# Optimization experiments

Hardware: AMD Instinct MI355X
Metric: run time of the kernel (lower is better)

The kernel has to match this reference:

```python
import jax, jax.numpy as jnp
import numpy as np
import math

B, S, D, H, C, A, SD, L, STEPS = 128, 256, 1024, 16, 50, 32, 64, 6, 10


def setup_inputs():
    key = jax.random.key(0)
    ks = jax.random.split(key, 16)
    rn = lambda k, sh, std=0.02: jax.random.normal(k, sh, jnp.float32) * std
    z = lambda sh: jnp.zeros(sh, jnp.float32)
    o = lambda sh: jnp.ones(sh, jnp.float32)
    return dict(
        reasoning=jax.random.normal(ks[0], (B, S, D), jnp.float32),
        state=jax.random.normal(ks[1], (B, SD), jnp.float32),
        x0=jax.random.normal(ks[2], (B, C, A), jnp.float32),
        W_se=rn(ks[3], (SD, D)), b_se=z(D), g_se=o(D), be_se=z(D),
        W_ap=rn(ks[4], (A, D)), b_ap=z(D),
        W_ad=rn(ks[5], (D, A), 0.001), b_ad=z(A),
        mem_latent=rn(ks[6], (1, 1, D)),
        Wq=rn(ks[7], (D, D)), bq=z(D), Wk=rn(ks[8], (D, D)), bk=z(D),
        Wv=rn(ks[9], (D, D)), bv=z(D), Wo=rn(ks[10], (D, D)), bo=z(D),
        g_q=o(D), be_q=z(D), g_kv=o(D), be_kv=z(D),
        W_fp=rn(ks[11], (D, D)), b_fp=z(D),
        pos_emb=rn(ks[12], (C, D)),
        filmW=rn(ks[13], (L, D, D)), filmb=z((L, D)), filmg=o((L, D)), filmbe=z((L, D)),
        filmWf=rn(ks[14], (L, D, 2 * D)), filmbf=z((L, 2 * D)),
        flow_steps=STEPS,
    )


def _ln(x, g, b):
    m = x.mean(-1, keepdims=True)
    v = jnp.mean((x - m) ** 2, -1, keepdims=True)
    return (x - m) * jax.lax.rsqrt(v + 1e-5) * g + b


def reference(reasoning, state, x0, W_se, b_se, g_se, be_se, W_ap, b_ap, W_ad, b_ad,
              mem_latent, Wq, bq, Wk, bk, Wv, bv, Wo, bo, g_q, be_q, g_kv, be_kv,
              W_fp, b_fp, pos_emb, filmW, filmb, filmg, filmbe, filmWf, filmbf, flow_steps):
    B_, C_, A_ = x0.shape
    D_ = W_ap.shape[1]
    dh = D_ // H
    # --- generate_mem: cross-attn from learned latent over [reasoning; state_enc] ---
    se = _ln(state @ W_se + b_se, g_se, be_se)[:, None, :]          # [B,1,D]
    kv = _ln(jnp.concatenate([reasoning, se], 1), g_kv, be_kv)      # [B,S+1,D]
    q = _ln(jnp.broadcast_to(mem_latent, (B_, 1, D_)), g_q, be_q)   # [B,1,D]
    qh = (q @ Wq + bq).reshape(B_, 1, H, dh)
    kh = (kv @ Wk + bk).reshape(B_, -1, H, dh)
    vh = (kv @ Wv + bv).reshape(B_, -1, H, dh)
    att = jax.nn.softmax(jnp.einsum('bqhd,bkhd->bhqk', qh, kh) / math.sqrt(dh), -1)
    mem = jnp.einsum('bhqk,bkhd->bqhd', att, vh).reshape(B_, 1, D_) @ Wo + bo
    film_vec = mem[:, 0] @ W_fp + b_fp                               # [B,D]
    cond = jnp.broadcast_to(film_vec[:, None, :], (B_, C_, D_)).reshape(B_ * C_, D_)
    half = D_ // 2
    freqs = jnp.exp(jnp.linspace(0.0, math.log(1000.0), half))

    def velocity(x_t, t):
        x = x_t @ W_ap + b_ap + pos_emb[None]                        # [B,C,D]
        targ = t[:, None] * freqs[None, :]
        temb = jnp.concatenate([jnp.sin(targ), jnp.cos(targ)], -1)   # [B,D]
        h = (x + temb[:, None, :]).reshape(B_ * C_, D_)

        def film_step(h, p):
            W, b, g, be, Wf, bf = p
            hh = _ln(h @ W + b, g, be)
            gamma, beta = jnp.split(cond @ Wf + bf, 2, -1)
            return jax.nn.gelu((1.0 + gamma) * hh + beta, approximate=False), None

        h, _ = jax.lax.scan(film_step, h, (filmW, filmb, filmg, filmbe, filmWf, filmbf))
        return (h @ W_ad + b_ad).reshape(B_, C_, A_)

    # --- flow-matching Euler integration (sample) ---
    dt = 1.0 / flow_steps
    ts = jnp.arange(flow_steps, dtype=jnp.float32) * dt

    def euler(x_t, tval):
        v = velocity(x_t, jnp.full((B_,), tval))
        return x_t + v * dt, None

    x_t, _ = jax.lax.scan(euler, x0, ts)
    return x_t
```

## Files before the change

### kernel.cpp

```cpp
#include <hip/hip_runtime.h>
#include <math.h>

#define NB 128
#define NS 256
#define ND 1024
#define NH 16
#define NC 50
#define NA 32
#define NSD 64
#define NL 6
#define NSTEPS 10
#define NM (NB*NC)
#define NKV (NS+1)

typedef unsigned short u16;
typedef short bf16x8 __attribute__((ext_vector_type(8)));
typedef float f32x4 __attribute__((ext_vector_type(4)));
typedef unsigned short us4 __attribute__((ext_vector_type(4)));
typedef unsigned short us8 __attribute__((ext_vector_type(8)));

typedef __attribute__((address_space(1))) const void* gas_p;
typedef __attribute__((address_space(3))) void* las_p;

__device__ __forceinline__ float b2f(u16 h) { return __uint_as_float(((unsigned int)h) << 16); }
__device__ __forceinline__ u16 f2b(float f) {
  unsigned int u = __float_as_uint(f);
  return (u16)((u + 0x7fffu + ((u >> 16) & 1u)) >> 16);
}
__device__ __forceinline__ void gld16(const void* g, void* l) {
  __builtin_amdgcn_global_load_lds((gas_p)g, (las_p)l, 16, 0, 0);
}

__device__ __forceinline__ float wredsum(float v) {
#pragma unroll
  for (int o = 32; o > 0; o >>= 1) v += __shfl_down(v, o, 64);
  return v;
}
__device__ __forceinline__ void bsum2(float& a, float& b, float* red, int t) {
  float ra = wredsum(a), rb = wredsum(b);
  if ((t & 63) == 0) { red[(t >> 6) * 2] = ra; red[(t >> 6) * 2 + 1] = rb; }
  __syncthreads();
  a = red[0] + red[2] + red[4] + red[6];
  b = red[1] + red[3] + red[5] + red[7];
  __syncthreads();
}

__global__ __launch_bounds__(512) void film_gemm(const u16* __restrict__ Ag,
                                                 const u16* __restrict__ Bg,
                                                 u16* __restrict__ Ug) {
  __shared__ u16 As[2][4096];
  __shared__ u16 Bs[2][4096];
  const int t = threadIdx.x, lane = t & 63, w = t >> 6;
  const int rb_ = blockIdx.x;
  const int bid = (rb_ & 7) * 50 + (rb_ >> 3);
  const int tm = bid >> 3, tn = bid & 7;
  const u16* Ab = Ag + (size_t)tm * 128 * ND;
  const u16* Bb = Bg + (size_t)tn * 128 * ND;
  const int srow = t >> 2, sq = (t & 3) * 8;
  const int wm = w >> 2, wn = w & 3;
  const int wr = wm * 64, wc = wn * 32;
  const int fr = lane & 15, fq = (lane >> 4) * 8;

  f32x4 acc[4][2];
#pragma unroll
  for (int m = 0; m < 4; ++m)
#pragma unroll
    for (int n = 0; n < 2; ++n)
#pragma unroll
      for (int j = 0; j < 4; ++j) acc[m][n][j] = 0.f;

  gld16(Ab + (size_t)srow * ND + sq, As[0] + w * 512);
  gld16(Bb + (size_t)srow * ND + sq, Bs[0] + w * 512);
  __syncthreads();

  for (int it = 0; it < 32; ++it) {
    const int cur = it & 1;
    if (it < 31) {
      const int k0 = (it + 1) * 32;
      gld16(Ab + (size_t)srow * ND + k0 + sq, As[cur ^ 1] + w * 512);
      gld16(Bb + (size_t)srow * ND + k0 + sq, Bs[cur ^ 1] + w * 512);
    }
    bf16x8 af[4], bfv[2];
#pragma unroll
    for (int m = 0; m < 4; ++m) af[m] = *(const bf16x8*)(As[cur] + (wr + m * 16 + fr) * 32 + fq);
#pragma unroll
    for (int n = 0; n < 2; ++n) bfv[n] = *(const bf16x8*)(Bs[cur] + (wc + n * 16 + fr) * 32 + fq);
#pragma unroll
    for (int m = 0; m < 4; ++m)
#pragma unroll
      for (int n = 0; n < 2; ++n)
        acc[m][n] = __builtin_amdgcn_mfma_f32_16x16x32_bf16(af[m], bfv[n], acc[m][n], 0, 0, 0);
    __syncthreads();
  }
  const int rbb = tm * 128 + wr + (lane >> 4) * 4;
  const int cbb = tn * 128 + wc + fr;
#pragma unroll
  for (int m = 0; m < 4; ++m)
#pragma unroll
    for (int n = 0; n < 2; ++n)
#pragma unroll
      for (int j = 0; j < 4; ++j)
        Ug[(size_t)(rbb + m * 16 + j) * ND + cbb + n * 16] = f2b(acc[m][n][j]);
}

__global__ __launch_bounds__(256) void bgemm(const u16* __restrict__ A, const int a_rstride,
    const int a_zoff, const u16* __restrict__ Bp, const long long b_zoff,
    const float* __restrict__ bias, const int bias_zoff, u16* __restrict__ C,
    const int c_rstride, const long long c_zoff) {
  __shared__ u16 As[4096];
  __shared__ u16 Bs[2048];
  const int t = threadIdx.x, wv = t >> 6, lane = t & 63;
  const int nt = blockIdx.x, z = blockIdx.y;
  const u16* Ab = A + (size_t)z * a_zoff;
  const u16* Bb = Bp + (size_t)z * b_zoff + (size_t)nt * 64 * ND;
  const int ca = wv * 128 + lane;
  const int ra0 = ca >> 2, qa0 = (ca & 3) * 8;
  const int ca1 = ca + 64;
  const int ra1 = ca1 >> 2, qa1 = (ca1 & 3) * 8;
  const int cbk = wv * 64 + lane;
  const int rb0 = cbk >> 2, qb0 = (cbk & 3) * 8;
  const int wr = (wv >> 1) * 64, wc = (wv & 1) * 32;
  const int fr = lane & 15, fq = (lane >> 4) * 8;

  f32x4 acc[4][2];
#pragma unroll
  for (int m = 0; m < 4; ++m)
#pragma unroll
    for (int n = 0; n < 2; ++n)
#pragma unroll
      for (int j = 0; j < 4; ++j) acc[m][n][j] = 0.f;

  for (int k0 = 0; k0 < ND; k0 += 32) {
    __syncthreads();
    gld16(Ab + (size_t)ra0 * a_rstride + k0 + qa0, As + wv * 1024);
    gld16(Ab + (size_t)ra1 * a_rstride + k0 + qa1, As + wv * 1024 + 512);
    gld16(Bb + (size_t)rb0 * ND + k0 + qb0, Bs + wv * 512);
    __syncthreads();
    bf16x8 af[4], bfv[2];
#pragma unroll
    for (int m = 0; m < 4; ++m) af[m] = *(const bf16x8*)(As + (wr + m * 16 + fr) * 32 + fq);
#pragma unroll
    for (int n = 0; n < 2; ++n) bfv[n] = *(const bf16x8*)(Bs + (wc + n * 16 + fr) * 32 + fq);
#pragma unroll
    for (int m = 0; m < 4; ++m)
#pragma unroll
      for (int n = 0; n < 2; ++n)
        acc[m][n] = __builtin_amdgcn_mfma_f32_16x16x32_bf16(af[m], bfv[n], acc[m][n], 0, 0, 0);
  }
  const int rb = wr + (lane >> 4) * 4;
#pragma unroll
  for (int n = 0; n < 2; ++n) {
    const int col = nt * 64 + wc + n * 16 + fr;
    const float bz = bias[(size_t)z * bias_zoff + col];
#pragma unroll
    for (int m = 0; m < 4; ++m)
#pragma unroll
      for (int j = 0; j < 4; ++j)
        C[(size_t)z * c_zoff + (size_t)(rb + m * 16 + j) * c_rstride + col] =
            f2b(acc[m][n][j] + bz);
  }
}

__global__ __launch_bounds__(256) void ln_film(const u16* __restrict__ U,
    const float* __restrict__ lb, const float* __restrict__ lg, const float* __restrict__ lbe,
    const u16* __restrict__ gbB, u16* __restrict__ Hout) {
  const int t = threadIdx.x, wv = t >> 6, lane = t & 63;
  const int row = blockIdx.x * 4 + wv;
  const int b = row / NC;
  const int d0 = lane * 16;
  const u16* up = U + (size_t)row * ND + d0;
  us8 u0 = *(const us8*)up;
  us8 u1 = *(const us8*)(up + 8);
  float lbv[16], lgv[16], lbev[16];
#pragma unroll
  for (int i = 0; i < 4; ++i) {
    *(f32x4*)&lbv[i * 4]  = *(const f32x4*)&lb[d0 + i * 4];
    *(f32x4*)&lgv[i * 4]  = *(const f32x4*)&lg[d0 + i * 4];
    *(f32x4*)&lbev[i * 4] = *(const f32x4*)&lbe[d0 + i * 4];
  }
  float x[16];
#pragma unroll
  for (int i = 0; i < 8; ++i) x[i] = b2f((u16)u0[i]) + lbv[i];
#pragma unroll
  for (int i = 0; i < 8; ++i) x[8 + i] = b2f((u16)u1[i]) + lbv[8 + i];
  float s = 0.f, q = 0.f;
#pragma unroll
  for (int i = 0; i < 16; ++i) { s += x[i]; q += x[i] * x[i]; }
#pragma unroll
  for (int o = 32; o > 0; o >>= 1) { s += __shfl_xor(s, o, 64); q += __shfl_xor(q, o, 64); }
  const float m = s * (1.f / ND);
  const float rstd = rsqrtf(q * (1.f / ND) - m * m + 1e-5f);
  const u16* gbb = gbB + (size_t)b * (2 * ND);
  us8 g0 = *(const us8*)(gbb + d0);
  us8 g1 = *(const us8*)(gbb + d0 + 8);
  us8 e0 = *(const us8*)(gbb + ND + d0);
  us8 e1 = *(const us8*)(gbb + ND + d0 + 8);
  us8 o0, o1;
#pragma unroll
  for (int i = 0; i < 16; ++i) {
    const float hh = (x[i] - m) * rstd * lgv[i] + lbev[i];
    const float ga = (i < 8) ? b2f((u16)g0[i]) : b2f((u16)g1[i - 8]);
    const float be = (i < 8) ? b2f((u16)e0[i]) : b2f((u16)e1[i - 8]);
    const float y = (1.f + ga) * hh + be;
    const float gl = 0.5f * y * (1.f + erff(y * 0.70710678118654752f));
    const u16 r = f2b(gl);
    if (i < 8) o0[i] = r; else o1[i - 8] = r;
  }
  u16* op = Hout + (size_t)row * ND + d0;
  *(us8*)op = o0;
  *(us8*)(op + 8) = o1;
}

__global__ __launch_bounds__(256) void h0_mfma(const float* __restrict__ X,
    const u16* __restrict__ WapP, const float* __restrict__ bt,
    const float* __restrict__ pos, u16* __restrict__ Hout) {
  __shared__ u16 As[4096];
  __shared__ u16 Bs[4096];
  const int t = threadIdx.x, wv = t >> 6, lane = t & 63;
  const int r0 = blockIdx.x * 128, c0 = blockIdx.y * 128;
  {
    const int r = t >> 1, hh = (t & 1) * 16;
    const float* xp = X + (size_t)(r0 + r) * NA + hh;
    u16* ad = As + r * 32 + hh;
#pragma unroll
    for (int i = 0; i < 4; ++i) {
      const f32x4 v = *(const f32x4*)(xp + i * 4);
      us4 o;
#pragma unroll
      for (int j = 0; j < 4; ++j) o[j] = f2b(v[j]);
      *(us4*)(ad + i * 4) = o;
    }
  }
  const u16* Bb = WapP + (size_t)c0 * NA;
  {
    const int c = wv * 128 + lane;
    gld16(Bb + (size_t)(c >> 2) * NA + (c & 3) * 8, Bs + wv * 1024);
    const int c1 = c + 64;
    gld16(Bb + (size_t)(c1 >> 2) * NA + (c1 & 3) * 8, Bs + wv * 1024 + 512);
  }
  __syncthreads();
  const int wr = (wv >> 1) * 64, wc = (wv & 1) * 64;
  const int fr = lane & 15, fq = (lane >> 4) * 8;
  bf16x8 af[4], bfv[4];
#pragma unroll
  for (int m = 0; m < 4; ++m) af[m] = *(const bf16x8*)(As + (wr + m * 16 + fr) * 32 + fq);
#pragma unroll
  for (int n = 0; n < 4; ++n) bfv[n] = *(const bf16x8*)(Bs + (wc + n * 16 + fr) * 32 + fq);
  f32x4 acc[4][4];
#pragma unroll
  for (int m = 0; m < 4; ++m)
#pragma unroll
    for (int n = 0; n < 4; ++n) {
#pragma unroll
      for (int j = 0; j < 4; ++j) acc[m][n][j] = 0.f;
      acc[m][n] = __builtin_amdgcn_mfma_f32_16x16x32_bf16(af[m], bfv[n], acc[m][n], 0, 0, 0);
    }
#pragma unroll
  for (int n = 0; n < 4; ++n) {
    const int col = c0 + wc + n * 16 + fr;
    const float btv = bt[col];
#pragma unroll
    for (int m = 0; m < 4; ++m)
#pragma unroll
      for (int j = 0; j < 4; ++j) {
        const int gr = r0 + wr + m * 16 + (lane >> 4) * 4 + j;
        const int c = gr % NC;
        Hout[(size_t)gr * ND + col] = f2b(acc[m][n][j] + btv + pos[(size_t)c * ND + col]);
      }
  }
}

__global__ __launch_bounds__(256) void vx_kernel(const u16* __restrict__ Hf,
    const u16* __restrict__ WadP, const float* __restrict__ b_ad,
    const float* __restrict__ Xin, float* __restrict__ Xout) {
  const int t = threadIdx.x, wv = t >> 6, lane = t & 63;
  const int r0 = blockIdx.x * 64 + wv * 16;
  f32x4 a0, a1;
#pragma unroll
  for (int j = 0; j < 4; ++j) { a0[j] = 0.f; a1[j] = 0.f; }
  const u16* ap = Hf + (size_t)(r0 + (lane & 15)) * ND + (lane >> 4) * 8;
  const u16* bp = WadP + lane * 8;
#pragma unroll 4
  for (int kt = 0; kt < 32; ++kt) {
    bf16x8 av = *(const bf16x8*)(ap + kt * 32);
    bf16x8 w0 = *(const bf16x8*)(bp + (kt * 2 + 0) * 512);
    bf16x8 w1 = *(const bf16x8*)(bp + (kt * 2 + 1) * 512);
    a0 = __builtin_amdgcn_mfma_f32_16x16x32_bf16(av, w0, a0, 0, 0, 0);
    a1 = __builtin_amdgcn_mfma_f32_16x16x32_bf16(av, w1, a1, 0, 0, 0);
  }
  const int rr = r0 + (lane >> 4) * 4;
  const int c0 = lane & 15;
#pragma unroll
  for (int j = 0; j < 4; ++j) {
    const int row = rr + j;
    const int i0 = row * NA + c0;
    Xout[i0] = Xin[i0] + 0.1f * (a0[j] + b_ad[c0]);
    const int i1 = row * NA + 16 + c0;
    Xout[i1] = Xin[i1] + 0.1f * (a1[j] + b_ad[16 + c0]);
  }
}

__global__ __launch_bounds__(256) void packT(const float* __restrict__ src,
    const long long src_zoff, const int srcw, u16* __restrict__ dst,
    const long long dst_zoff) {
  __shared__ float tl[64 * 65];
  const int l = blockIdx.z, kt = blockIdx.y, nt = blockIdx.x;
  const int t = threadIdx.x;
  const float* s = src + (size_t)l * src_zoff + (size_t)(kt * 64) * srcw + nt * 64;
#pragma unroll
  for (int j = 0; j < 4; ++j) {
    const int f = (t + j * 256) * 4;
    const int r = f >> 6, c = f & 63;
    const f32x4 v = *(const f32x4*)&s[(size_t)r * srcw + c];
#pragma unroll
    for (int i = 0; i < 4; ++i) tl[r * 65 + c + i] = v[i];
  }
  __syncthreads();
  const int nn = t >> 2, kg = (t & 3) * 16;
  us8 o0, o1;
#pragma unroll
  for (int i = 0; i < 8; ++i) o0[i] = f2b(tl[(kg + i) * 65 + nn]);
#pragma unroll
  for (int i = 0; i < 8; ++i) o1[i] = f2b(tl[(kg + 8 + i) * 65 + nn]);
  u16* d = dst + (size_t)l * dst_zoff + (size_t)(nt * 64 + nn) * ND + kt * 64 + kg;
  *(us8*)d = o0;
  *(us8*)(d + 8) = o1;
}

__global__ __launch_bounds__(256) void prep_misc(const float* __restrict__ W_ap,
    const float* __restrict__ W_ad, u16* __restrict__ WapP, u16* __restrict__ WadP,
    const float* __restrict__ b_ap, float* __restrict__ bt) {
  const int id = blockIdx.x * 256 + threadIdx.x;
#pragma unroll
  for (int i = 0; i < 4; ++i) {
    const int e = id * 4 + i;
    const int n = e >> 5, k = e & 31;
    WapP[e] = f2b(W_ap[k * ND + n]);
  }
#pragma unroll
  for (int i = 0; i < 4; ++i) {
    const int e = id * 4 + i;
    const int kt = e >> 10, rem = e & 1023;
    const int at = rem >> 9, rem2 = rem & 511;
    const int ln = rem2 >> 3, j = rem2 & 7;
    const int k = kt * 32 + (ln >> 4) * 8 + j;
    const int col = at * 16 + (ln & 15);
    WadP[e] = f2b(W_ad[k * NA + col]);
  }
  if (id < 2560) {
#pragma unroll
    for (int i = 0; i < 4; ++i) {
      const int e = id * 4 + i;
      const int s = e >> 10, d = e & 1023;
      const double lam = 6.907755278982137 / 511.0;
      const double tt = 0.1 * (double)s;
      double v;
      if (d < 512) v = sin(tt * exp(lam * (double)d));
      else         v = cos(tt * exp(lam * (double)(d - 512)));
      bt[e] = (float)v + b_ap[d];
    }
  }
}

__global__ __launch_bounds__(256) void se_kernel(const float* __restrict__ state,
    const float* __restrict__ W_se, const float* __restrict__ b_se,
    const float* __restrict__ g_se, const float* __restrict__ be_se,
    float* __restrict__ se_d) {
  __shared__ float xs[NSD];
  __shared__ float red[8];
  const int b = blockIdx.x, t = threadIdx.x;
  if (t < NSD) xs[t] = state[b * NSD + t];
  __syncthreads();
  const int d0 = t * 4;
  float acc[4];
#pragma unroll
  for (int i = 0; i < 4; ++i) acc[i] = b_se[d0 + i];
  for (int k = 0; k < NSD; ++k) {
    const float xv = xs[k];
    const f32x4 wv = *(const f32x4*)&W_se[(size_t)k * ND + d0];
#pragma unroll
    for (int i = 0; i < 4; ++i) acc[i] += xv * wv[i];
  }
  float s = acc[0] + acc[1] + acc[2] + acc[3];
  float q = acc[0]*acc[0] + acc[1]*acc[1] + acc[2]*acc[2] + acc[3]*acc[3];
  bsum2(s, q, red, t);
  const float m = s * (1.f / ND);
  const float rstd = rsqrtf(q * (1.f / ND) - m * m + 1e-5f);
#pragma unroll
  for (int i = 0; i < 4; ++i)
    se_d[(size_t)b * ND + d0 + i] = (acc[i] - m) * rstd * g_se[d0 + i] + be_se[d0 + i];
}

__global__ __launch_bounds__(256) void q1_kernel(const float* __restrict__ lat,
    const float* __restrict__ g_q, const float* __restrict__ be_q, float* __restrict__ qn) {
  __shared__ float red[8];
  const int t = threadIdx.x;
  const int d0 = t * 4;
  const f32x4 x = *(const f32x4*)&lat[d0];
  float s = x[0] + x[1] + x[2] + x[3];
  float q = x[0]*x[0] + x[1]*x[1] + x[2]*x[2] + x[3]*x[3];
  bsum2(s, q, red, t);
  const float m = s * (1.f / ND);
  const float rstd = rsqrtf(q * (1.f / ND) - m * m + 1e-5f);
#pragma unroll
  for (int i = 0; i < 4; ++i)
    qn[d0 + i] = (x[i] - m) * rstd * g_q[d0 + i] + be_q[d0 + i];
}

__global__ __launch_bounds__(256) void q2_split(const float* __restrict__ qn,
    const float* __restrict__ Wq, float* __restrict__ part) {
  __shared__ float ql[64];
  const int cc = blockIdx.x, kc = blockIdx.y, t = threadIdx.x;
  if (t < 64) ql[t] = qn[kc * 64 + t];
  __syncthreads();
  const int c = cc * 256 + t;
  float acc = 0.f;
#pragma unroll 8
  for (int k = 0; k < 64; ++k) acc += ql[k] * Wq[(size_t)(kc * 64 + k) * ND + c];
  part[kc * ND + c] = acc;
}
__global__ __launch_bounds__(256) void q2_red(const float* __restrict__ part,
    const float* __restrict__ bq, float* __restrict__ qh) {
  const int c = blockIdx.x * 256 + threadIdx.x;
  float a = bq[c];
#pragma unroll
  for (int i = 0; i < 16; ++i) a += part[i * ND + c];
  qh[c] = a;
}

__global__ __launch_bounds__(256) void q3_kernel(const float* __restrict__ Wk,
    const float* __restrict__ bk, const float* __restrict__ qh,
    float* __restrict__ wTf, float* __restrict__ sb) {
  __shared__ float ql[ND];
  __shared__ float wl[4 * ND];
  const int t = threadIdx.x;
  *(f32x4*)&ql[t * 4] = *(const f32x4*)&qh[t * 4];
  const int d0 = blockIdx.x * 4;
  const float* src = Wk + (size_t)d0 * ND;
#pragma unroll
  for (int i = 0; i < 4; ++i)
    *(f32x4*)&wl[(i * 256 + t) * 4] = *(const f32x4*)&src[(size_t)(i * 256 + t) * 4];
  __syncthreads();
  if (t < 64) {
    const int dl = t >> 4, h = t & 15;
    const float* wr_ = wl + dl * ND + h * 64;
    const float* qr = ql + h * 64;
    float acc = 0.f;
#pragma unroll 8
    for (int j = 0; j < 64; ++j) acc += wr_[j] * qr[j];
    wTf[h * ND + d0 + dl] = acc * 0.125f;
  } else if (blockIdx.x == 0 && t >= 64 && t < 80) {
    const int h = t - 64;
    float sv = 0.f;
    for (int j = 0; j < 64; ++j) sv += bk[h * 64 + j] * ql[h * 64 + j];
    sb[h] = sv * 0.125f;
  }
}

__global__ __launch_bounds__(256) void q4_kernel(const float* __restrict__ wTf,
    const float* __restrict__ g_kv, const float* __restrict__ be_kv,
    const float* __restrict__ sb, float* __restrict__ gwF, float* __restrict__ cgw,
    float* __restrict__ cbw) {
  __shared__ float red[8];
  const int h = blockIdx.x, t = threadIdx.x;
  float pg = 0.f, pb = 0.f;
  for (int d = t; d < ND; d += 256) {
    const float w = wTf[h * ND + d];
    const float gw = g_kv[d] * w;
    gwF[h * ND + d] = gw;
    pg += gw;
    pb += be_kv[d] * w;
  }
  bsum2(pg, pb, red, t);
  if (t == 0) { cgw[h] = pg; cbw[h] = pb + sb[h]; }
}

__global__ __launch_bounds__(256) void scores2(const float* __restrict__ reasoning,
    const float* __restrict__ se_d, const float* __restrict__ gwF,
    const float* __restrict__ cgw, const float* __restrict__ cbw,
    float* __restrict__ scores, float* __restrict__ stats) {
  __shared__ float gwl[8 * ND];
  const int t = threadIdx.x, wv = t >> 6, lane = t & 63;
  const int r = blockIdx.x * 4 + wv;
  const int b = r / NKV, k = r - b * NKV;
  const float* src = (k < NS) ? reasoning + ((size_t)b * NS + k) * ND
                              : se_d + (size_t)b * ND;
  float x[16];
#pragma unroll
  for (int i = 0; i < 4; ++i) {
    const f32x4 v = *(const f32x4*)(src + i * 256 + lane * 4);
#pragma unroll
    for (int j = 0; j < 4; ++j) x[i * 4 + j] = v[j];
  }
  float s = 0.f, q = 0.f;
#pragma unroll
  for (int i = 0; i < 16; ++i) { s += x[i]; q += x[i] * x[i]; }
#pragma unroll
  for (int o = 32; o > 0; o >>= 1) { s += __shfl_xor(s, o, 64); q += __shfl_xor(q, o, 64); }
  const float m = s * (1.f / ND);
  const float rstd = rsqrtf(q * (1.f / ND) - m * m + 1e-5f);
  if (lane == 0) {
    stats[(size_t)r * 2] = m;
    stats[(size_t)r * 2 + 1] = rstd;
  }
#pragma unroll
  for (int ph = 0; ph < 2; ++ph) {
    if (ph) __syncthreads();
    for (int f = t; f < 2048; f += 256)
      *(f32x4*)&gwl[f * 4] = *(const f32x4*)&gwF[(size_t)ph * 8 * ND + f * 4];
    __syncthreads();
    float acc[8];
#pragma unroll
    for (int h = 0; h < 8; ++h) acc[h] = 0.f;
#pragma unroll
    for (int i = 0; i < 4; ++i) {
#pragma unroll
      for (int h = 0; h < 8; ++h) {
        const f32x4 w4 = *(const f32x4*)&gwl[h * ND + i * 256 + lane * 4];
        acc[h] += x[i*4+0]*w4[0] + x[i*4+1]*w4[1] + x[i*4+2]*w4[2] + x[i*4+3]*w4[3];
      }
    }
#pragma unroll
    for (int o = 32; o > 0; o >>= 1)
#pragma unroll
      for (int h = 0; h < 8; ++h) acc[h] += __shfl_xor(acc[h], o, 64);
    if (lane < 8) {
      float out = 0.f;
#pragma unroll
      for (int h = 0; h < 8; ++h) if (lane == h) out = acc[h];
      const int hh = ph * 8 + lane;
      scores[((size_t)b * NH + hh) * NKV + k] = rstd * out - rstd * m * cgw[hh] + cbw[hh];
    }
  }
}

__global__ __launch_bounds__(256) void ctx2(const float* __restrict__ reasoning,
    const float* __restrict__ se_d, const float* __restrict__ scores,
    const float* __restrict__ stats, const float* __restrict__ g_kv,
    const float* __restrict__ be_kv, u16* __restrict__ ctxb) {
  __shared__ float sc[NH][260];
  __shared__ float stm[NKV], str[NKV];
  __shared__ float c1s[NH];
  const int chunk = blockIdx.x, b = blockIdx.y;
  const int t = threadIdx.x, wv = t >> 6, lane = t & 63;
#pragma unroll
  for (int h = 0; h < NH; ++h)
    for (int k = t; k < NKV; k += 256) sc[h][k] = scores[((size_t)b * NH + h) * NKV + k];
  for (int k = t; k < NKV; k += 256) {
    stm[k] = stats[((size_t)b * NKV + k) * 2];
    str[k] = stats[((size_t)b * NKV + k) * 2 + 1];
  }
  __syncthreads();
#pragma unroll
  for (int hh = 0; hh < 4; ++hh) {
    const int h = wv * 4 + hh;
    float mx = -1e30f;
    for (int i = 0; i < 5; ++i) { const int k = lane + i * 64; if (k < NKV) mx = fmaxf(mx, sc[h][k]); }
#pragma unroll
    for (int o = 32; o > 0; o >>= 1) mx = fmaxf(mx, __shfl_xor(mx, o, 64));
    float sm = 0.f;
    for (int i = 0; i < 5; ++i) {
      const int k = lane + i * 64;
      if (k < NKV) { const float e = __expf(sc[h][k] - mx); sc[h][k] = e; sm += e; }
    }
#pragma unroll
    for (int o = 32; o > 0; o >>= 1) sm += __shfl_xor(sm, o, 64);
    const float inv = 1.f / sm;
    float c1 = 0.f;
    for (int i = 0; i < 5; ++i) {
      const int k = lane + i * 64;
      if (k < NKV) {
        const float a = sc[h][k] * inv * str[k];
        sc[h][k] = a;
        c1 += a * stm[k];
      }
    }
#pragma unroll
    for (int o = 32; o > 0; o >>= 1) c1 += __shfl_xor(c1, o, 64);
    if (lane == 0) c1s[h] = c1;
  }
  __syncthreads();
  const int c = chunk * 256 + t;
  const float g = g_kv[c], be = be_kv[c];
  float acc[16];
#pragma unroll
  for (int h = 0; h < 16; ++h) acc[h] = 0.f;
  const float* xc = reasoning + (size_t)b * NS * ND + c;
#pragma unroll 2
  for (int k4 = 0; k4 < 64; ++k4) {
    const float x0 = xc[(size_t)(k4 * 4 + 0) * ND];
    const float x1 = xc[(size_t)(k4 * 4 + 1) * ND];
    const float x2 = xc[(size_t)(k4 * 4 + 2) * ND];
    const float x3 = xc[(size_t)(k4 * 4 + 3) * ND];
#pragma unroll
    for (int h = 0; h < 16; ++h) {
      const f32x4 w = *(const f32x4*)&sc[h][k4 * 4];
      acc[h] += w[0] * x0 + w[1] * x1 + w[2] * x2 + w[3] * x3;
    }
  }
  {
    const float xs = se_d[(size_t)b * ND + c];
#pragma unroll
    for (int h = 0; h < 16; ++h) acc[h] += sc[h][NS] * xs;
  }
#pragma unroll
  for (int h = 0; h < 16; ++h)
    ctxb[((size_t)b * NH + h) * ND + c] = f2b(g * (acc[h] - c1s[h]) + be);
}

extern "C" void kernel_launch(void* const* d_in, const int* in_sizes, int n_in,
                              void* d_out, int out_size, void* d_ws, size_t ws_size,
                              hipStream_t stream) {
  (void)in_sizes; (void)n_in; (void)out_size; (void)ws_size;
  const float* reasoning = (const float*)d_in[0];
  const float* state  = (const float*)d_in[1];
  const float* x0     = (const float*)d_in[2];
  const float* W_se   = (const float*)d_in[3];
  const float* b_se   = (const float*)d_in[4];
  const float* g_se   = (const float*)d_in[5];
  const float* be_se  = (const float*)d_in[6];
  const float* W_ap   = (const float*)d_in[7];
  const float* b_ap   = (const float*)d_in[8];
  const float* W_ad   = (const float*)d_in[9];
  const float* b_ad   = (const float*)d_in[10];
  const float* mem_latent = (const float*)d_in[11];
  const float* Wq = (const float*)d_in[12]; const float* bq = (const float*)d_in[13];
  const float* Wk = (const float*)d_in[14]; const float* bk = (const float*)d_in[15];
  const float* Wv = (const float*)d_in[16]; const float* bv = (const float*)d_in[17];
  const float* Wo = (const float*)d_in[18]; const float* bo = (const float*)d_in[19];
  const float* g_q  = (const float*)d_in[20]; const float* be_q  = (const float*)d_in[21];
  const float* g_kv = (const float*)d_in[22]; const float* be_kv = (const float*)d_in[23];
  const float* W_fp = (const float*)d_in[24]; const float* b_fp = (const float*)d_in[25];
  const float* pos_emb = (const float*)d_in[26];
  const float* filmW  = (const float*)d_in[27]; const float* filmb  = (const float*)d_in[28];
  const float* filmg  = (const float*)d_in[29]; const float* filmbe = (const float*)d_in[30];
  const float* filmWf = (const float*)d_in[31]; const float* filmbf = (const float*)d_in[32];

  char* base = (char*)d_ws;
  size_t off = 0;
  auto alloc = [&](size_t bytes) -> void* {
    void* p = base + off;
    off += (bytes + 255) & ~(size_t)255;
    return p;
  };
  u16*  Wpack   = (u16*)alloc((size_t)NL * ND * ND * 2);
  u16*  Wfp2    = (u16*)alloc((size_t)NL * 2 * ND * ND * 2);
  u16*  Wvp     = (u16*)alloc((size_t)ND * ND * 2);
  u16*  Wop     = (u16*)alloc((size_t)ND * ND * 2);
  u16*  Wfpp    = (u16*)alloc((size_t)ND * ND * 2);
  u16*  WapP    = (u16*)alloc((size_t)NA * ND * 2);
  u16*  WadP    = (u16*)alloc((size_t)32768 * 2);
  float* bt     = (float*)alloc((size_t)NSTEPS * ND * 4);
  float* se_d   = (float*)alloc((size_t)NB * ND * 4);
  float* qn     = (float*)alloc((size_t)ND * 4);
  float* qh     = (float*)alloc((size_t)ND * 4);
  float* part   = (float*)alloc((size_t)16 * ND * 4);
  float* wTf    = (float*)alloc((size_t)NH * ND * 4);
  float* sb     = (float*)alloc((size_t)NH * 4);
  float* gwF    = (float*)alloc((size_t)NH * ND * 4);
  float* cgw    = (float*)alloc((size_t)NH * 4);
  float* cbw    = (float*)alloc((size_t)NH * 4);
  float* stats  = (float*)alloc((size_t)NB * NKV * 2 * 4);
  float* scores = (float*)alloc((size_t)NB * NH * NKV * 4);
  u16*  ctxb    = (u16*)alloc((size_t)NB * NH * ND * 2);
  u16*  mem_pre = (u16*)alloc((size_t)NB * ND * 2);
  u16*  memb    = (u16*)alloc((size_t)NB * ND * 2);
  u16*  fvb     = (u16*)alloc((size_t)NB * ND * 2);
  u16*  gbB     = (u16*)alloc((size_t)NL * NB * 2 * ND * 2);
  u16*  hbuf    = (u16*)alloc((size_t)NM * ND * 2);
  u16*  ubuf    = (u16*)alloc((size_t)NM * ND * 2);

  packT<<<dim3(16, 16, NL), 256, 0, stream>>>(filmW, (long long)ND * ND, ND, Wpack,
                                              (long long)ND * ND);
  packT<<<dim3(32, 16, NL), 256, 0, stream>>>(filmWf, (long long)ND * 2 * ND, 2 * ND, Wfp2,
                                              (long long)2 * ND * ND);
  packT<<<dim3(16, 16, 1), 256, 0, stream>>>(Wv, 0, ND, Wvp, 0);
  packT<<<dim3(16, 16, 1), 256, 0, stream>>>(Wo, 0, ND, Wop, 0);
  packT<<<dim3(16, 16, 1), 256, 0, stream>>>(W_fp, 0, ND, Wfpp, 0);
  prep_misc<<<32, 256, 0, stream>>>(W_ap, W_ad, WapP, WadP, b_ap, bt);

  se_kernel<<<NB, 256, 0, stream>>>(state, W_se, b_se, g_se, be_se, se_d);
  q1_kernel<<<1, 256, 0, stream>>>(mem_latent, g_q, be_q, qn);
  q2_split<<<dim3(4, 16), 256, 0, stream>>>(qn, Wq, part);
  q2_red<<<4, 256, 0, stream>>>(part, bq, qh);
  q3_kernel<<<256, 256, 0, stream>>>(Wk, bk, qh, wTf, sb);
  q4_kernel<<<NH, 256, 0, stream>>>(wTf, g_kv, be_kv, sb, gwF, cgw, cbw);
  scores2<<<(NB * NKV) / 4, 256, 0, stream>>>(reasoning, se_d, gwF, cgw, cbw, scores, stats);
  ctx2<<<dim3(4, NB), 256, 0, stream>>>(reasoning, se_d, scores, stats, g_kv, be_kv, ctxb);
  bgemm<<<dim3(1, 16), 256, 0, stream>>>(ctxb, NH * ND, ND, Wvp, (long long)64 * ND, bv, 64,
                                         mem_pre, ND, 64);
  bgemm<<<dim3(16, 1), 256, 0, stream>>>(mem_pre, ND, 0, Wop, 0, bo, 0, memb, ND, 0);
  bgemm<<<dim3(16, 1), 256, 0, stream>>>(memb, ND, 0, Wfpp, 0, b_fp, 0, fvb, ND, 0);
  bgemm<<<dim3(32, NL), 256, 0, stream>>>(fvb, ND, 0, Wfp2, (long long)2 * ND * ND, filmbf,
                                          2 * ND, gbB, 2 * ND, (long long)NB * 2 * ND);

  for (int s = 0; s < NSTEPS; ++s) {
    const float* xin = (s == 0) ? x0 : (const float*)d_out;
    h0_mfma<<<dim3(NM / 128, 8), 256, 0, stream>>>(xin, WapP, bt + (size_t)s * ND, pos_emb,
                                                   hbuf);
    for (int l = 0; l < NL; ++l) {
      film_gemm<<<400, 512, 0, stream>>>(hbuf, Wpack + (size_t)l * ND * ND, ubuf);
      ln_film<<<NM / 4, 256, 0, stream>>>(ubuf, filmb + (size_t)l * ND, filmg + (size_t)l * ND,
                                          filmbe + (size_t)l * ND,
                                          gbB + (size_t)l * NB * 2 * ND, hbuf);
    }
    vx_kernel<<<NM / 64, 256, 0, stream>>>(hbuf, WadP, b_ad, xin, (float*)d_out);
  }
}
```

Measured before the change: 2.825 ms.

## Deepen FiLM GEMM K-tile with swizzled LDS and move attention scores to MFMA

The FiLM GEMM now stages 64-wide K tiles with an XOR-swizzled LDS layout, which halves the number of barrier iterations and reduces LDS bank conflicts. Its epilogue goes through shared memory so the output is written as coalesced 16-byte stores instead of scattered 2-byte writes. The attention score kernel is rewritten to use bf16 MFMA against a prepacked bf16 copy of the folded key-projection weights, with each block handling 64 rows. This trades some precision in the scores for fewer scalar FMAs and less weight reloading, and doubles the LDS footprint of the GEMM, which may lower occupancy.

```diff
diff --git a/kernel.cpp b/kernel.cpp
--- a/kernel.cpp
+++ b/kernel.cpp
@@ -48,18 +48,20 @@
 __global__ __launch_bounds__(512) void film_gemm(const u16* __restrict__ Ag,
                                                  const u16* __restrict__ Bg,
                                                  u16* __restrict__ Ug) {
-  __shared__ u16 As[2][4096];
-  __shared__ u16 Bs[2][4096];
+  __shared__ u16 As[2][8192];
+  __shared__ u16 Bs[2][8192];
   const int t = threadIdx.x, lane = t & 63, w = t >> 6;
   const int rb_ = blockIdx.x;
   const int bid = (rb_ & 7) * 50 + (rb_ >> 3);
   const int tm = bid >> 3, tn = bid & 7;
   const u16* Ab = Ag + (size_t)tm * 128 * ND;
   const u16* Bb = Bg + (size_t)tn * 128 * ND;
-  const int srow = t >> 2, sq = (t & 3) * 8;
+  const int c0 = t, c1 = t + 512;
+  const int sr0 = c0 >> 3, sq0 = (c0 & 7) ^ (sr0 & 7);
+  const int sr1 = c1 >> 3, sq1 = (c1 & 7) ^ (sr1 & 7);
   const int wm = w >> 2, wn = w & 3;
   const int wr = wm * 64, wc = wn * 32;
-  const int fr = lane & 15, fq = (lane >> 4) * 8;
+  const int fr = lane & 15, f8 = lane >> 4, r7 = fr & 7;
 
   f32x4 acc[4][2];
 #pragma unroll
@@ -69,38 +71,57 @@
 #pragma unroll
       for (int j = 0; j < 4; ++j) acc[m][n][j] = 0.f;
 
-  gld16(Ab + (size_t)srow * ND + sq, As[0] + w * 512);
-  gld16(Bb + (size_t)srow * ND + sq, Bs[0] + w * 512);
-  __syncthreads();
-
-  for (int it = 0; it < 32; ++it) {
+#define STAGE_FG(buf, k0)                                              \
+  gld16(Ab + (size_t)sr0 * ND + (k0) + sq0 * 8, As[buf] + w * 512);    \
+  gld16(Ab + (size_t)sr1 * ND + (k0) + sq1 * 8, As[buf] + 4096 + w * 512); \
+  gld16(Bb + (size_t)sr0 * ND + (k0) + sq0 * 8, Bs[buf] + w * 512);    \
+  gld16(Bb + (size_t)sr1 * ND + (k0) + sq1 * 8, Bs[buf] + 4096 + w * 512);
+
+  STAGE_FG(0, 0)
+  __syncthreads();
+
+  for (int it = 0; it < 16; ++it) {
     const int cur = it & 1;
-    if (it < 31) {
-      const int k0 = (it + 1) * 32;
-      gld16(Ab + (size_t)srow * ND + k0 + sq, As[cur ^ 1] + w * 512);
-      gld16(Bb + (size_t)srow * ND + k0 + sq, Bs[cur ^ 1] + w * 512);
-    }
-    bf16x8 af[4], bfv[2];
-#pragma unroll
-    for (int m = 0; m < 4; ++m) af[m] = *(const bf16x8*)(As[cur] + (wr + m * 16 + fr) * 32 + fq);
-#pragma unroll
-    for (int n = 0; n < 2; ++n) bfv[n] = *(const bf16x8*)(Bs[cur] + (wc + n * 16 + fr) * 32 + fq);
-#pragma unroll
-    for (int m = 0; m < 4; ++m)
-#pragma unroll
-      for (int n = 0; n < 2; ++n)
-        acc[m][n] = __builtin_amdgcn_mfma_f32_16x16x32_bf16(af[m], bfv[n], acc[m][n], 0, 0, 0);
+    if (it < 15) { STAGE_FG(cur ^ 1, (it + 1) * 64) }
+#pragma unroll
+    for (int ks = 0; ks < 2; ++ks) {
+      const int qp = (ks * 4 + f8);
+      bf16x8 af[4], bfv[2];
+#pragma unroll
+      for (int m = 0; m < 4; ++m) {
+        const int row = wr + m * 16 + fr;
+        af[m] = *(const bf16x8*)(As[cur] + row * 64 + (qp ^ r7) * 8);
+      }
+#pragma unroll
+      for (int n = 0; n < 2; ++n) {
+        const int row = wc + n * 16 + fr;
+        bfv[n] = *(const bf16x8*)(Bs[cur] + row * 64 + (qp ^ r7) * 8);
+      }
+#pragma unroll
+      for (int m = 0; m < 4; ++m)
+#pragma unroll
+        for (int n = 0; n < 2; ++n)
+          acc[m][n] = __builtin_amdgcn_mfma_f32_16x16x32_bf16(af[m], bfv[n], acc[m][n], 0, 0, 0);
+    }
     __syncthreads();
   }
-  const int rbb = tm * 128 + wr + (lane >> 4) * 4;
-  const int cbb = tn * 128 + wc + fr;
+#undef STAGE_FG
+  u16* Cs = &As[0][0];
 #pragma unroll
   for (int m = 0; m < 4; ++m)
 #pragma unroll
     for (int n = 0; n < 2; ++n)
 #pragma unroll
       for (int j = 0; j < 4; ++j)
-        Ug[(size_t)(rbb + m * 16 + j) * ND + cbb + n * 16] = f2b(acc[m][n][j]);
+        Cs[(wr + m * 16 + f8 * 4 + j) * 128 + wc + n * 16 + fr] = f2b(acc[m][n][j]);
+  __syncthreads();
+  {
+    const int row = t >> 2, cb0 = (t & 3) * 32;
+    u16* dst = Ug + (size_t)(tm * 128 + row) * ND + tn * 128 + cb0;
+    const u16* srcl = Cs + row * 128 + cb0;
+#pragma unroll
+    for (int i = 0; i < 4; ++i) *(us8*)(dst + i * 8) = *(const us8*)(srcl + i * 8);
+  }
 }
 
 __global__ __launch_bounds__(256) void bgemm(const u16* __restrict__ A, const int a_rstride,
@@ -459,7 +480,7 @@
 
 __global__ __launch_bounds__(256) void q4_kernel(const float* __restrict__ wTf,
     const float* __restrict__ g_kv, const float* __restrict__ be_kv,
-    const float* __restrict__ sb, float* __restrict__ gwF, float* __restrict__ cgw,
+    const float* __restrict__ sb, u16* __restrict__ gwP, float* __restrict__ cgw,
     float* __restrict__ cbw) {
   __shared__ float red[8];
   const int h = blockIdx.x, t = threadIdx.x;
@@ -467,7 +488,7 @@
   for (int d = t; d < ND; d += 256) {
     const float w = wTf[h * ND + d];
     const float gw = g_kv[d] * w;
-    gwF[h * ND + d] = gw;
+    gwP[(d >> 5) * 512 + (h + 16 * ((d >> 3) & 3)) * 8 + (d & 7)] = f2b(gw);
     pg += gw;
     pb += be_kv[d] * w;
   }
@@ -475,62 +496,62 @@
   if (t == 0) { cgw[h] = pg; cbw[h] = pb + sb[h]; }
 }
 
-__global__ __launch_bounds__(256) void scores2(const float* __restrict__ reasoning,
-    const float* __restrict__ se_d, const float* __restrict__ gwF,
+__global__ __launch_bounds__(256) void scores3(const float* __restrict__ reasoning,
+    const float* __restrict__ se_d, const u16* __restrict__ gwP,
     const float* __restrict__ cgw, const float* __restrict__ cbw,
     float* __restrict__ scores, float* __restrict__ stats) {
-  __shared__ float gwl[8 * ND];
+  __shared__ u16 gwl[16384];
+  __shared__ float smv[4][16], srv[4][16];
   const int t = threadIdx.x, wv = t >> 6, lane = t & 63;
-  const int r = blockIdx.x * 4 + wv;
-  const int b = r / NKV, k = r - b * NKV;
-  const float* src = (k < NS) ? reasoning + ((size_t)b * NS + k) * ND
-                              : se_d + (size_t)b * ND;
-  float x[16];
-#pragma unroll
-  for (int i = 0; i < 4; ++i) {
-    const f32x4 v = *(const f32x4*)(src + i * 256 + lane * 4);
-#pragma unroll
-    for (int j = 0; j < 4; ++j) x[i * 4 + j] = v[j];
-  }
+#pragma unroll
+  for (int i = 0; i < 8; ++i)
+    gld16(gwP + (i * 256 + t) * 8, gwl + i * 2048 + wv * 512);
+  const int r0 = blockIdx.x * 64 + wv * 16;
+  const int rowA = r0 + (lane & 15);
+  const unsigned bA = (unsigned)rowA / NKV;
+  const int kA = rowA - bA * NKV;
+  const float* ptr = ((kA < NS) ? reasoning + ((size_t)bA * NS + kA) * ND
+                                : se_d + (size_t)bA * ND) + (lane >> 4) * 8;
+  __syncthreads();
+  f32x4 acc;
+#pragma unroll
+  for (int j = 0; j < 4; ++j) acc[j] = 0.f;
   float s = 0.f, q = 0.f;
-#pragma unroll
-  for (int i = 0; i < 16; ++i) { s += x[i]; q += x[i] * x[i]; }
-#pragma unroll
-  for (int o = 32; o > 0; o >>= 1) { s += __shfl_xor(s, o, 64); q += __shfl_xor(q, o, 64); }
+  for (int kt = 0; kt < 32; ++kt) {
+    const f32x4 v0 = *(const f32x4*)(ptr + kt * 32);
+    const f32x4 v1 = *(const f32x4*)(ptr + kt * 32 + 4);
+    bf16x8 af;
+#pragma unroll
+    for (int j = 0; j < 4; ++j) {
+      af[j] = (short)f2b(v0[j]);
+      af[4 + j] = (short)f2b(v1[j]);
+      s += v0[j] + v1[j];
+      q += v0[j] * v0[j] + v1[j] * v1[j];
+    }
+    const bf16x8 bfr = *(const bf16x8*)(gwl + kt * 512 + lane * 8);
+    acc = __builtin_amdgcn_mfma_f32_16x16x32_bf16(af, bfr, acc, 0, 0, 0);
+  }
+  s += __shfl_xor(s, 16, 64); s += __shfl_xor(s, 32, 64);
+  q += __shfl_xor(q, 16, 64); q += __shfl_xor(q, 32, 64);
   const float m = s * (1.f / ND);
   const float rstd = rsqrtf(q * (1.f / ND) - m * m + 1e-5f);
-  if (lane == 0) {
-    stats[(size_t)r * 2] = m;
-    stats[(size_t)r * 2 + 1] = rstd;
-  }
-#pragma unroll
-  for (int ph = 0; ph < 2; ++ph) {
-    if (ph) __syncthreads();
-    for (int f = t; f < 2048; f += 256)
-      *(f32x4*)&gwl[f * 4] = *(const f32x4*)&gwF[(size_t)ph * 8 * ND + f * 4];
-    __syncthreads();
-    float acc[8];
-#pragma unroll
-    for (int h = 0; h < 8; ++h) acc[h] = 0.f;
-#pragma unroll
-    for (int i = 0; i < 4; ++i) {
-#pragma unroll
-      for (int h = 0; h < 8; ++h) {
-        const f32x4 w4 = *(const f32x4*)&gwl[h * ND + i * 256 + lane * 4];
-        acc[h] += x[i*4+0]*w4[0] + x[i*4+1]*w4[1] + x[i*4+2]*w4[2] + x[i*4+3]*w4[3];
-      }
-    }
-#pragma unroll
-    for (int o = 32; o > 0; o >>= 1)
-#pragma unroll
-      for (int h = 0; h < 8; ++h) acc[h] += __shfl_xor(acc[h], o, 64);
-    if (lane < 8) {
-      float out = 0.f;
-#pragma unroll
-      for (int h = 0; h < 8; ++h) if (lane == h) out = acc[h];
-      const int hh = ph * 8 + lane;
-      scores[((size_t)b * NH + hh) * NKV + k] = rstd * out - rstd * m * cgw[hh] + cbw[hh];
-    }
+  if (lane < 16) {
+    smv[wv][lane] = m; srv[wv][lane] = rstd;
+    const int row = r0 + lane;
+    stats[(size_t)row * 2] = m;
+    stats[(size_t)row * 2 + 1] = rstd;
+  }
+  __syncthreads();
+  const int h = lane & 15;
+  const float cg = cgw[h], cb = cbw[h];
+#pragma unroll
+  for (int j = 0; j < 4; ++j) {
+    const int lr = (lane >> 4) * 4 + j;
+    const int row = r0 + lr;
+    const float mm = smv[wv][lr], rr = srv[wv][lr];
+    const unsigned b = (unsigned)row / NKV;
+    const int k = row - b * NKV;
+    scores[((size_t)b * NH + h) * NKV + k] = rr * acc[j] - rr * mm * cg + cb;
   }
 }
 
@@ -657,7 +678,7 @@
   float* part   = (float*)alloc((size_t)16 * ND * 4);
   float* wTf    = (float*)alloc((size_t)NH * ND * 4);
   float* sb     = (float*)alloc((size_t)NH * 4);
-  float* gwF    = (float*)alloc((size_t)NH * ND * 4);
+  u16*  gwP     = (u16*)alloc((size_t)NH * ND * 2);
   float* cgw    = (float*)alloc((size_t)NH * 4);
   float* cbw    = (float*)alloc((size_t)NH * 4);
   float* stats  = (float*)alloc((size_t)NB * NKV * 2 * 4);
@@ -684,8 +705,8 @@
   q2_split<<<dim3(4, 16), 256, 0, stream>>>(qn, Wq, part);
   q2_red<<<4, 256, 0, stream>>>(part, bq, qh);
   q3_kernel<<<256, 256, 0, stream>>>(Wk, bk, qh, wTf, sb);
-  q4_kernel<<<NH, 256, 0, stream>>>(wTf, g_kv, be_kv, sb, gwF, cgw, cbw);
-  scores2<<<(NB * NKV) / 4, 256, 0, stream>>>(reasoning, se_d, gwF, cgw, cbw, scores, stats);
+  q4_kernel<<<NH, 256, 0, stream>>>(wTf, g_kv, be_kv, sb, gwP, cgw, cbw);
+  scores3<<<(NB * NKV) / 64, 256, 0, stream>>>(reasoning, se_d, gwP, cgw, cbw, scores, stats);
   ctx2<<<dim3(4, NB), 256, 0, stream>>>(reasoning, se_d, scores, stats, g_kv, be_kv, ctxb);
   bgemm<<<dim3(1, 16), 256, 0, stream>>>(ctxb, NH * ND, ND, Wvp, (long long)64 * ND, bv, 64,
                                          mem_pre, ND, 64);
```

Result: faster. 2.590 ms (-8.3%).
